# Optimization experiments

Hardware: AMD Instinct MI355X
Metric: run time of the kernel (lower is better)

## Reference

```python
import jax, jax.numpy as jnp
import numpy as np

OUT, IN, GS = 11008, 4096, 128   # out_features, in_features, group_size
G = IN // GS                     # num_groups = 32 (in_features divisible by group_size)
TOKENS = 8192                    # batch 4 * seq 2048


def setup_inputs() -> dict:
    key = jax.random.key(0)
    k1, k2, k3, k4, k5 = jax.random.split(key, 5)
    x = jax.random.normal(k1, (TOKENS, IN), dtype=jnp.float32)
    # packed int4 weights: two nibbles per byte, stored as int32 in [0,256)
    qweight = jax.random.randint(k2, (OUT, IN // 2), 0, 256, dtype=jnp.int32)
    # realistic GPTQ scales (small positive) and zero-points in [0,15]
    scales = jax.random.uniform(k3, (OUT, G), dtype=jnp.float32) * 0.01 + 1e-3
    zeros = jax.random.uniform(k4, (OUT, G), dtype=jnp.float32) * 15.0
    bias = jax.random.normal(k5, (OUT,), dtype=jnp.float32) * 0.01
    return {"x": x, "qweight": qweight, "scales": scales, "zeros": zeros, "bias": bias}


def _dequant(qweight, scales, zeros):
    # unpack: column 2i = low nibble, column 2i+1 = high nibble (matches torch loop)
    low = (qweight & 15).astype(jnp.float32)          # [OUT, IN/2]
    high = ((qweight >> 4) & 15).astype(jnp.float32)  # [OUT, IN/2]
    w = jnp.stack([low, high], axis=-1).reshape(OUT, IN)
    # group-wise dequant: (q - zero) * scale per group of GS input channels
    w = (w.reshape(OUT, G, GS) - zeros[:, :, None]) * scales[:, :, None]
    return w.reshape(OUT, IN)


def reference(x, qweight, scales, zeros, bias):
    w = _dequant(qweight, scales, zeros)   # [OUT, IN] fp32
    # F.linear: x @ w.T + bias
    return jnp.einsum('ti,oi->to', x, w) + bias
```

## Files before the change

### kernel.cpp

```cpp
#include <hip/hip_runtime.h>
#include <stdint.h>

#define OUTF 11008
#define INF  4096
#define NG   32
#define TOK  8192
#define KB4  2048

#define BM 256
#define BN 256
#define BK 64
#define NT (INF / BK)
#define GX (OUTF / BN)
#define GY (TOK / BM)
#define NWG (GX * GY)

typedef unsigned short u16;
typedef __attribute__((ext_vector_type(8))) short bf16x8;
typedef __attribute__((ext_vector_type(4))) float f32x4;

__device__ inline u16 f2bf(float f) {
  union { float f; uint32_t u; } v; v.f = f;
  return (u16)((v.u + 0x7fff + ((v.u >> 16) & 1)) >> 16);
}

__device__ inline void async_copy16(const void* g, const void* l) {
  __builtin_amdgcn_global_load_lds(
      (__attribute__((address_space(1))) void*)(g),
      (__attribute__((address_space(3))) void*)(l), 16, 0, 0);
}

#define FENCE() asm volatile("" ::: "memory")
#define BAR()   do { FENCE(); __builtin_amdgcn_s_barrier(); FENCE(); } while (0)
#define VMCNT(n) asm volatile("s_waitcnt vmcnt(" #n ")" ::: "memory")
#define LGKM0()  asm volatile("s_waitcnt lgkmcnt(0)" ::: "memory")


__global__ void dequant_w(const int* __restrict__ QW, const float* __restrict__ scales,
                          const float* __restrict__ zeros, u16* __restrict__ Wb) {
  const int idx = blockIdx.x * 256 + threadIdx.x;
  const int e = idx * 8;
  const int o = e >> 11;
  const int c = e & (KB4 - 1);
  const int g = c >> 6;
  const float s = scales[o * NG + g];
  const float z = zeros[o * NG + g];
  const float zs = -z * s;
#pragma unroll
  for (int h = 0; h < 2; ++h) {
    const int4 q = *(const int4*)(QW + (size_t)o * KB4 + c + h * 4);
    const int qq[4] = {q.x, q.y, q.z, q.w};
    union { u16 t[8]; int4 v; } u;
#pragma unroll
    for (int j = 0; j < 4; ++j) {
      u.t[2 * j]     = f2bf(fmaf((float)(qq[j] & 15), s, zs));
      u.t[2 * j + 1] = f2bf(fmaf((float)((qq[j] >> 4) & 15), s, zs));
    }
    *(int4*)(Wb + (size_t)o * INF + 2 * (c + h * 4)) = u.v;
  }
}

__global__ void cvt_x(const float* __restrict__ X, u16* __restrict__ Xb) {
  const size_t base = ((size_t)blockIdx.x * 256 + threadIdx.x) * 16;
#pragma unroll
  for (int h = 0; h < 2; ++h) {
    const float4 a = *(const float4*)(X + base + h * 8);
    const float4 b = *(const float4*)(X + base + h * 8 + 4);
    union { u16 t[8]; int4 v; } u;
    u.t[0] = f2bf(a.x); u.t[1] = f2bf(a.y); u.t[2] = f2bf(a.z); u.t[3] = f2bf(a.w);
    u.t[4] = f2bf(b.x); u.t[5] = f2bf(b.y); u.t[6] = f2bf(b.z); u.t[7] = f2bf(b.w);
    *(int4*)(Xb + base + h * 8) = u.v;
  }
}


__global__ __launch_bounds__(512, 2) void gemm_pre512(const u16* __restrict__ A,
                                                      const u16* __restrict__ B,
                                                      const float* __restrict__ bias,
                                                      float* __restrict__ C) {
  __shared__ __align__(16) u16 As[2][BM * BK];
  __shared__ __align__(16) u16 Bs[2][BN * BK];
  const int tid = threadIdx.x;
  const int lane = tid & 63;
  const int wid = __builtin_amdgcn_readfirstlane(tid >> 6);

  const int lin = blockIdx.x;
  const int wg = (lin & 7) * (NWG / 8) + (lin >> 3);
  const int bm = wg / GX;
  const int bn = wg % GX;

  const u16* Ab = A + (size_t)bm * BM * INF;
  const u16* Bb = B + (size_t)bn * BN * INF;

  const int rowoff = tid >> 3;
  const int gran = (tid & 7) ^ (rowoff & 7);
  const u16* Asrc = Ab + (size_t)rowoff * INF + gran * 8;
  const u16* Bsrc = Bb + (size_t)rowoff * INF + gran * 8;
  const int wid8 = wid * 8;

  const int rr = lane & 15;
  const int q4 = lane >> 4;
  const int wm = wid >> 2;
  const int wn = wid & 3;

  f32x4 acc[8][4] = {};
  bf16x8 af[4];
  bf16x8 bfv[4];

#define STAGE1(LDS, SRC, TT, R0)                                               \
  async_copy16((SRC) + (size_t)(R0) * INF + (size_t)(TT) * BK,                 \
               (const char*)(LDS) + ((R0) + wid8) * 128);

#define PH_READ_A(S, KS, MH)                                                   \
  _Pragma("unroll") for (int mi = 0; mi < 4; ++mi)                             \
    af[mi] = *(const bf16x8*)&As[S][(wm * 128 + ((MH) * 4 + mi) * 16 + rr) *   \
                                        BK +                                   \
                                    ((((KS) * 4 + q4) ^ (rr & 7)) * 8)];

#define PH_READ_B(S, KS)                                                       \
  _Pragma("unroll") for (int ni = 0; ni < 4; ++ni)                             \
    bfv[ni] = *(const bf16x8*)&Bs[S][(wn * 64 + ni * 16 + rr) * BK +           \
                                     ((((KS) * 4 + q4) ^ (rr & 7)) * 8)];

#define PH_MFMA(MH)                                                            \
  do {                                                                         \
    __builtin_amdgcn_s_setprio(1);                                             \
    _Pragma("unroll") for (int mi = 0; mi < 4; ++mi)                           \
      _Pragma("unroll") for (int ni = 0; ni < 4; ++ni)                         \
        acc[(MH) * 4 + mi][ni] = __builtin_amdgcn_mfma_f32_16x16x32_bf16(      \
            af[mi], bfv[ni], acc[(MH) * 4 + mi][ni], 0, 0, 0);                 \
    __builtin_amdgcn_s_setprio(0);                                             \
  } while (0)

#define TILE(S, T)                                                             \
  do {                                                                         \
                                                            \
    PH_READ_A(S, 0, 0); PH_READ_B(S, 0);                                       \
    if ((T) + 1 < NT) {                                                        \
      STAGE1(&As[(S) ^ 1][0], Asrc, (T) + 1, 64)                               \
      STAGE1(&As[(S) ^ 1][0], Asrc, (T) + 1, 192)                              \
    }                                                                          \
    BAR(); LGKM0(); PH_MFMA(0); BAR();                                         \
                                                            \
    PH_READ_A(S, 0, 1);                                                        \
    BAR(); LGKM0(); PH_MFMA(1); BAR();                                         \
                                                            \
    PH_READ_A(S, 1, 0); PH_READ_B(S, 1);                                       \
    BAR(); LGKM0(); PH_MFMA(0); BAR();                                         \
                                                            \
    PH_READ_A(S, 1, 1);                                                        \
    if ((T) + 2 < NT) {                                                        \
      STAGE1(&As[S][0], Asrc, (T) + 2, 0)                                      \
      STAGE1(&As[S][0], Asrc, (T) + 2, 128)                                    \
      STAGE1(&Bs[S][0], Bsrc, (T) + 2, 0)                                      \
      STAGE1(&Bs[S][0], Bsrc, (T) + 2, 64)                                     \
      STAGE1(&Bs[S][0], Bsrc, (T) + 2, 128)                                    \
      STAGE1(&Bs[S][0], Bsrc, (T) + 2, 192)                                    \
      VMCNT(6);                                                                \
    } else {                                                                   \
      VMCNT(0);                                                                \
    }                                                                          \
    BAR(); LGKM0(); PH_MFMA(1); BAR();                                         \
  } while (0)

  STAGE1(&As[0][0], Asrc, 0, 0)   STAGE1(&As[0][0], Asrc, 0, 64)
  STAGE1(&As[0][0], Asrc, 0, 128) STAGE1(&As[0][0], Asrc, 0, 192)
  STAGE1(&Bs[0][0], Bsrc, 0, 0)   STAGE1(&Bs[0][0], Bsrc, 0, 64)
  STAGE1(&Bs[0][0], Bsrc, 0, 128) STAGE1(&Bs[0][0], Bsrc, 0, 192)
  STAGE1(&As[1][0], Asrc, 1, 0)   STAGE1(&As[1][0], Asrc, 1, 128)
  STAGE1(&Bs[1][0], Bsrc, 1, 0)   STAGE1(&Bs[1][0], Bsrc, 1, 64)
  STAGE1(&Bs[1][0], Bsrc, 1, 128) STAGE1(&Bs[1][0], Bsrc, 1, 192)
  VMCNT(6);
  BAR();

  for (int t = 0; t < NT; t += 2) {
    TILE(0, t);
    TILE(1, t + 1);
  }

  const int ncol = lane & 15;
  const int qrow = (lane >> 4) * 4;
  float bv[4];
#pragma unroll
  for (int ni = 0; ni < 4; ++ni)
    bv[ni] = bias[bn * BN + wn * 64 + ni * 16 + ncol];
#pragma unroll
  for (int mi = 0; mi < 8; ++mi)
#pragma unroll
    for (int ni = 0; ni < 4; ++ni) {
      const int gn = bn * BN + wn * 64 + ni * 16 + ncol;
#pragma unroll
      for (int r = 0; r < 4; ++r) {
        const int gm = bm * BM + wm * 128 + mi * 16 + qrow + r;
        C[(size_t)gm * OUTF + gn] = acc[mi][ni][r] + bv[ni];
      }
    }
}


#define FBM 128
#define FBN 128

#define FMFMA_COMPUTE()                                                       \
  do {                                                                        \
    const int frr = lane & 15;                                                \
    const int fq4 = lane >> 4;                                                \
    _Pragma("unroll") for (int ks = 0; ks < 2; ++ks) {                        \
      bf16x8 fa[4], fb[4];                                                    \
      const int kk = (((ks * 4 + fq4) ^ (frr & 7)) * 8);                      \
      _Pragma("unroll") for (int i = 0; i < 4; ++i) {                         \
        fa[i] = *(const bf16x8*)&Asf[(mwave + i * 16 + frr) * BK + kk];       \
        fb[i] = *(const bf16x8*)&Bsf[(nwave + i * 16 + frr) * BK + kk];       \
      }                                                                       \
      _Pragma("unroll") for (int mi = 0; mi < 4; ++mi)                        \
        _Pragma("unroll") for (int ni = 0; ni < 4; ++ni)                      \
          facc[mi][ni] = __builtin_amdgcn_mfma_f32_16x16x32_bf16(             \
              fa[mi], fb[ni], facc[mi][ni], 0, 0, 0);                         \
    }                                                                         \
  } while (0)

__global__ __launch_bounds__(256) void gemm_fused(const float* __restrict__ X,
                                                  const int* __restrict__ QW,
                                                  const float* __restrict__ scales,
                                                  const float* __restrict__ zeros,
                                                  const float* __restrict__ bias,
                                                  float* __restrict__ C) {
  __shared__ __align__(16) u16 Asf[FBM * BK];
  __shared__ __align__(16) u16 Bsf[FBN * BK];
  const int tid = threadIdx.x;
  const int lane = tid & 63;
  const int wid = tid >> 6;
  const int bm = blockIdx.y, bn = blockIdx.x;
  const int row = tid >> 1;
  const int half = tid & 1;
  const float* xr = X + (size_t)(bm * FBM + row) * INF + half * 32;
  const int* qr = QW + (size_t)(bn * FBN + row) * KB4 + half * 16;
  const float* srow = scales + (size_t)(bn * FBN + row) * NG;
  const float* zrow = zeros + (size_t)(bn * FBN + row) * NG;
  const int mwave = (wid >> 1) * 64;
  const int nwave = (wid & 1) * 64;
  f32x4 facc[4][4] = {};

  for (int kb = 0; kb < INF / BK; ++kb) {
    const int k0 = kb * BK;
    union { u16 t[32]; int4 v[4]; } ta, tb;
#pragma unroll
    for (int j = 0; j < 8; ++j) {
      const float4 f = *(const float4*)(xr + k0 + j * 4);
      ta.t[4 * j]     = f2bf(f.x);
      ta.t[4 * j + 1] = f2bf(f.y);
      ta.t[4 * j + 2] = f2bf(f.z);
      ta.t[4 * j + 3] = f2bf(f.w);
    }
    {
      const float s = srow[kb >> 1];
      const float zs = -zrow[kb >> 1] * s;
#pragma unroll
      for (int j = 0; j < 4; ++j) {
        const int4 q = *(const int4*)(qr + kb * 32 + j * 4);
        const int qq[4] = {q.x, q.y, q.z, q.w};
#pragma unroll
        for (int u = 0; u < 4; ++u) {
          tb.t[8 * j + 2 * u]     = f2bf(fmaf((float)(qq[u] & 15), s, zs));
          tb.t[8 * j + 2 * u + 1] = f2bf(fmaf((float)((qq[u] >> 4) & 15), s, zs));
        }
      }
    }
    __syncthreads();
#pragma unroll
    for (int j = 0; j < 4; ++j) {
      *(int4*)&Asf[row * BK + (((half * 4 + j) ^ (row & 7)) * 8)] = ta.v[j];
      *(int4*)&Bsf[row * BK + (((half * 4 + j) ^ (row & 7)) * 8)] = tb.v[j];
    }
    __syncthreads();
    FMFMA_COMPUTE();
  }
  {
    const int ncol = lane & 15;
    const int qrow = (lane >> 4) * 4;
#pragma unroll
    for (int mi = 0; mi < 4; ++mi)
#pragma unroll
      for (int ni = 0; ni < 4; ++ni) {
        const int gn = bn * FBN + nwave + ni * 16 + ncol;
        const float bvv = bias[gn];
#pragma unroll
        for (int r = 0; r < 4; ++r) {
          const int gm = bm * FBM + mwave + mi * 16 + qrow + r;
          C[(size_t)gm * OUTF + gn] = facc[mi][ni][r] + bvv;
        }
      }
  }
}


extern "C" void kernel_launch(void* const* d_in, const int* in_sizes, int n_in,
                              void* d_out, int out_size, void* d_ws, size_t ws_size,
                              hipStream_t stream) {
  const float* x = (const float*)d_in[0];
  const int* qw = (const int*)d_in[1];
  const float* scales = (const float*)d_in[2];
  const float* zeros = (const float*)d_in[3];
  const float* bias = (const float*)d_in[4];
  float* out = (float*)d_out;

  const size_t needW = (size_t)OUTF * INF * sizeof(u16);
  const size_t needX = (size_t)TOK * INF * sizeof(u16);

  if (ws_size >= needW + needX) {
    u16* Wb = (u16*)d_ws;
    u16* Xb = (u16*)((char*)d_ws + needW);
    dequant_w<<<(OUTF * KB4 / 8) / 256, 256, 0, stream>>>(qw, scales, zeros, Wb);
    cvt_x<<<(TOK * INF / 16) / 256, 256, 0, stream>>>(x, Xb);
    gemm_pre512<<<dim3(NWG), 512, 0, stream>>>(Xb, Wb, bias, out);
  } else {
    gemm_fused<<<dim3(OUTF / FBN, FBM ? TOK / FBM : 1), 256, 0, stream>>>(x, qw, scales, zeros, bias, out);
  }
}
```

Measured before the change: 1.304 ms.

## Merge prep kernels and simplify GEMM pipeline to one barrier pair per tile

Replaces the separate weight-dequant and x-conversion kernels with a single grid-stride prep kernel, removing one launch. In the GEMM, the fine-grained four-phase schedule is dropped: it interleaved partial prefetches and barriers around each MFMA batch. The new schedule runs all MFMAs for a tile back to back, then issues the full prefetch of tile t+2 between two barriers. This cuts barrier count but may expose more global-load latency, since prefetch issue is delayed until compute on the buffer finishes.

```diff
diff --git a/kernel.cpp b/kernel.cpp
--- a/kernel.cpp
+++ b/kernel.cpp
@@ -33,43 +33,44 @@
 #define FENCE() asm volatile("" ::: "memory")
 #define BAR()   do { FENCE(); __builtin_amdgcn_s_barrier(); FENCE(); } while (0)
 #define VMCNT(n) asm volatile("s_waitcnt vmcnt(" #n ")" ::: "memory")
-#define LGKM0()  asm volatile("s_waitcnt lgkmcnt(0)" ::: "memory")
-
-
-__global__ void dequant_w(const int* __restrict__ QW, const float* __restrict__ scales,
-                          const float* __restrict__ zeros, u16* __restrict__ Wb) {
-  const int idx = blockIdx.x * 256 + threadIdx.x;
-  const int e = idx * 8;
-  const int o = e >> 11;
-  const int c = e & (KB4 - 1);
-  const int g = c >> 6;
-  const float s = scales[o * NG + g];
-  const float z = zeros[o * NG + g];
-  const float zs = -z * s;
-#pragma unroll
-  for (int h = 0; h < 2; ++h) {
-    const int4 q = *(const int4*)(QW + (size_t)o * KB4 + c + h * 4);
-    const int qq[4] = {q.x, q.y, q.z, q.w};
-    union { u16 t[8]; int4 v; } u;
-#pragma unroll
-    for (int j = 0; j < 4; ++j) {
-      u.t[2 * j]     = f2bf(fmaf((float)(qq[j] & 15), s, zs));
-      u.t[2 * j + 1] = f2bf(fmaf((float)((qq[j] >> 4) & 15), s, zs));
-    }
-    *(int4*)(Wb + (size_t)o * INF + 2 * (c + h * 4)) = u.v;
-  }
-}
-
-__global__ void cvt_x(const float* __restrict__ X, u16* __restrict__ Xb) {
-  const size_t base = ((size_t)blockIdx.x * 256 + threadIdx.x) * 16;
-#pragma unroll
-  for (int h = 0; h < 2; ++h) {
-    const float4 a = *(const float4*)(X + base + h * 8);
-    const float4 b = *(const float4*)(X + base + h * 8 + 4);
-    union { u16 t[8]; int4 v; } u;
-    u.t[0] = f2bf(a.x); u.t[1] = f2bf(a.y); u.t[2] = f2bf(a.z); u.t[3] = f2bf(a.w);
-    u.t[4] = f2bf(b.x); u.t[5] = f2bf(b.y); u.t[6] = f2bf(b.z); u.t[7] = f2bf(b.w);
-    *(int4*)(Xb + base + h * 8) = u.v;
+
+
+#define NXU ((long long)TOK * INF / 4)
+#define NWU ((long long)OUTF * KB4 / 4)
+#define PREPBLK 2048
+
+__global__ __launch_bounds__(256) void prep(const float* __restrict__ X,
+                                            const int* __restrict__ QW,
+                                            const float* __restrict__ scales,
+                                            const float* __restrict__ zeros,
+                                            u16* __restrict__ Xb,
+                                            u16* __restrict__ Wb) {
+  const long long stride = (long long)gridDim.x * 256;
+  for (long long i = (long long)blockIdx.x * 256 + threadIdx.x; i < NXU + NWU;
+       i += stride) {
+    if (i < NXU) {
+      const float4 f = ((const float4*)X)[i];
+      union { u16 t[4]; uint2 v; } u;
+      u.t[0] = f2bf(f.x); u.t[1] = f2bf(f.y);
+      u.t[2] = f2bf(f.z); u.t[3] = f2bf(f.w);
+      ((uint2*)Xb)[i] = u.v;
+    } else {
+      const long long j = i - NXU;
+      const int o = (int)(j >> 9);
+      const int c0 = ((int)j & 511) * 4;
+      const int g = c0 >> 6;
+      const float s = scales[o * NG + g];
+      const float zs = -zeros[o * NG + g] * s;
+      const int4 q = ((const int4*)QW)[j];
+      const int qq[4] = {q.x, q.y, q.z, q.w};
+      union { u16 t[8]; int4 v; } u;
+#pragma unroll
+      for (int k = 0; k < 4; ++k) {
+        u.t[2 * k]     = f2bf(fmaf((float)(qq[k] & 15), s, zs));
+        u.t[2 * k + 1] = f2bf(fmaf((float)((qq[k] >> 4) & 15), s, zs));
+      }
+      ((int4*)Wb)[j] = u.v;
+    }
   }
 }
 
@@ -111,6 +112,14 @@
   async_copy16((SRC) + (size_t)(R0) * INF + (size_t)(TT) * BK,                 \
                (const char*)(LDS) + ((R0) + wid8) * 128);
 
+#define STAGE_ALL(S, TT)                                                       \
+  do {                                                                         \
+    STAGE1(&As[S][0], Asrc, TT, 0)   STAGE1(&As[S][0], Asrc, TT, 64)           \
+    STAGE1(&As[S][0], Asrc, TT, 128) STAGE1(&As[S][0], Asrc, TT, 192)          \
+    STAGE1(&Bs[S][0], Bsrc, TT, 0)   STAGE1(&Bs[S][0], Bsrc, TT, 64)           \
+    STAGE1(&Bs[S][0], Bsrc, TT, 128) STAGE1(&Bs[S][0], Bsrc, TT, 192)          \
+  } while (0)
+
 #define PH_READ_A(S, KS, MH)                                                   \
   _Pragma("unroll") for (int mi = 0; mi < 4; ++mi)                             \
     af[mi] = *(const bf16x8*)&As[S][(wm * 128 + ((MH) * 4 + mi) * 16 + rr) *   \
@@ -134,43 +143,18 @@
 
 #define TILE(S, T)                                                             \
   do {                                                                         \
-                                                            \
-    PH_READ_A(S, 0, 0); PH_READ_B(S, 0);                                       \
-    if ((T) + 1 < NT) {                                                        \
-      STAGE1(&As[(S) ^ 1][0], Asrc, (T) + 1, 64)                               \
-      STAGE1(&As[(S) ^ 1][0], Asrc, (T) + 1, 192)                              \
-    }                                                                          \
-    BAR(); LGKM0(); PH_MFMA(0); BAR();                                         \
-                                                            \
-    PH_READ_A(S, 0, 1);                                                        \
-    BAR(); LGKM0(); PH_MFMA(1); BAR();                                         \
-                                                            \
-    PH_READ_A(S, 1, 0); PH_READ_B(S, 1);                                       \
-    BAR(); LGKM0(); PH_MFMA(0); BAR();                                         \
-                                                            \
-    PH_READ_A(S, 1, 1);                                                        \
-    if ((T) + 2 < NT) {                                                        \
-      STAGE1(&As[S][0], Asrc, (T) + 2, 0)                                      \
-      STAGE1(&As[S][0], Asrc, (T) + 2, 128)                                    \
-      STAGE1(&Bs[S][0], Bsrc, (T) + 2, 0)                                      \
-      STAGE1(&Bs[S][0], Bsrc, (T) + 2, 64)                                     \
-      STAGE1(&Bs[S][0], Bsrc, (T) + 2, 128)                                    \
-      STAGE1(&Bs[S][0], Bsrc, (T) + 2, 192)                                    \
-      VMCNT(6);                                                                \
-    } else {                                                                   \
-      VMCNT(0);                                                                \
-    }                                                                          \
-    BAR(); LGKM0(); PH_MFMA(1); BAR();                                         \
+    PH_READ_A(S, 0, 0); PH_READ_B(S, 0); PH_MFMA(0);                           \
+    PH_READ_A(S, 0, 1); PH_MFMA(1);                                            \
+    PH_READ_A(S, 1, 0); PH_READ_B(S, 1); PH_MFMA(0);                           \
+    PH_READ_A(S, 1, 1); PH_MFMA(1);                                            \
+    BAR();                                  \
+    if ((T) + 2 < NT) { STAGE_ALL(S, (T) + 2); VMCNT(8); } else { VMCNT(0); }  \
+    BAR();                         \
   } while (0)
 
-  STAGE1(&As[0][0], Asrc, 0, 0)   STAGE1(&As[0][0], Asrc, 0, 64)
-  STAGE1(&As[0][0], Asrc, 0, 128) STAGE1(&As[0][0], Asrc, 0, 192)
-  STAGE1(&Bs[0][0], Bsrc, 0, 0)   STAGE1(&Bs[0][0], Bsrc, 0, 64)
-  STAGE1(&Bs[0][0], Bsrc, 0, 128) STAGE1(&Bs[0][0], Bsrc, 0, 192)
-  STAGE1(&As[1][0], Asrc, 1, 0)   STAGE1(&As[1][0], Asrc, 1, 128)
-  STAGE1(&Bs[1][0], Bsrc, 1, 0)   STAGE1(&Bs[1][0], Bsrc, 1, 64)
-  STAGE1(&Bs[1][0], Bsrc, 1, 128) STAGE1(&Bs[1][0], Bsrc, 1, 192)
-  VMCNT(6);
+  STAGE_ALL(0, 0);
+  STAGE_ALL(1, 1);
+  VMCNT(8);
   BAR();
 
   for (int t = 0; t < NT; t += 2) {
@@ -310,10 +294,9 @@
   if (ws_size >= needW + needX) {
     u16* Wb = (u16*)d_ws;
     u16* Xb = (u16*)((char*)d_ws + needW);
-    dequant_w<<<(OUTF * KB4 / 8) / 256, 256, 0, stream>>>(qw, scales, zeros, Wb);
-    cvt_x<<<(TOK * INF / 16) / 256, 256, 0, stream>>>(x, Xb);
+    prep<<<PREPBLK, 256, 0, stream>>>(x, qw, scales, zeros, Xb, Wb);
     gemm_pre512<<<dim3(NWG), 512, 0, stream>>>(Xb, Wb, bias, out);
   } else {
-    gemm_fused<<<dim3(OUTF / FBN, FBM ? TOK / FBM : 1), 256, 0, stream>>>(x, qw, scales, zeros, bias, out);
-  }
-}
+    gemm_fused<<<dim3(OUTF / FBN, TOK / FBM), 256, 0, stream>>>(x, qw, scales, zeros, bias, out);
+  }
+}
```

Result: faster. 1.275 ms (-2.2%).
